# Kernel optimization log

Measured on AMD Instinct MI355X. Metric: run time of the kernel, lower is better.

## Reference

```python
import jax, jax.numpy as jnp
import numpy as np

N = 1024
D = 128  # hidden_dim
NEG = -1e9
LEAK = 0.2


def setup_inputs() -> dict:
    key = jax.random.key(0)
    ks = jax.random.split(key, 10)
    h = jax.random.normal(ks[0], (N, D), dtype=jnp.float32)
    adj = jax.random.randint(ks[1], (N, N), 0, 2, dtype=jnp.int32)  # 0/1 mask
    price_diff = jax.random.normal(ks[2], (N, N), dtype=jnp.float32)
    utilization = jax.random.uniform(ks[3], (N, N), dtype=jnp.float32)
    s = 0.05
    W = jax.random.normal(ks[4], (D, D), dtype=jnp.float32) * s          # W.weight [out,in]
    a = jax.random.normal(ks[5], (2 * D,), dtype=jnp.float32) * s        # attn.weight [1, 2D]
    W1 = jax.random.normal(ks[6], (D, D + 2), dtype=jnp.float32) * s     # mlp[0].weight [D, D+2]
    b1 = jnp.zeros((D,), dtype=jnp.float32)
    W2 = jax.random.normal(ks[7], (D, D), dtype=jnp.float32) * s         # mlp[2].weight [D, D]
    b2 = jnp.zeros((D,), dtype=jnp.float32)
    return {"h": h, "adj": adj, "price_diff": price_diff, "utilization": utilization,
            "W": W, "a": a, "W1": W1, "b1": b1, "W2": W2, "b2": b2}


def reference(h, adj, price_diff, utilization, W, a, W1, b1, W2, b2):
    # Linear projection (no bias): Wh = h @ W^T  -> [N, D]
    Wh = h @ W.T
    # GAT score: e_ij = leaky_relu(a^T [Wh_i || Wh_j]) = leaky_relu(s1_i + s2_j)
    s1 = Wh @ a[:D]          # [N]
    s2 = Wh @ a[D:]          # [N]
    e = jax.nn.leaky_relu(s1[:, None] + s2[None, :], LEAK)  # [N, N]
    mask = adj > 0
    e = jnp.where(mask, e, NEG)
    alpha = jax.nn.softmax(e, axis=-1) * mask.astype(e.dtype)  # zero rows with no neighbors
    # Edge MLP on [Wh_j || price_diff_ij || utilization_ij]
    W1h = W1[:, :D]          # [D, D] part acting on Wh_j
    w_pd = W1[:, D]          # [D]
    w_ut = W1[:, D + 1]      # [D]
    base = Wh @ W1h.T + b1   # [N, D], depends only on source node j
    m1 = jax.nn.relu(base[None, :, :]
                     + price_diff[:, :, None] * w_pd
                     + utilization[:, :, None] * w_ut)          # [N, N, D]
    m2 = m1 @ W2.T + b2                                          # [N, N, D]
    # Attention-weighted aggregation over neighbors j
    out = jnp.einsum('ij,ijd->id', alpha, m2)                    # [N, D]
    return out
```

## Files before the change

### kernel.cpp

```cpp
#include <hip/hip_runtime.h>
#include <hip/hip_bf16.h>

#define N 1024
#define D 128
#define LEAK 0.2f

#define MROWS 2

#define OFF_W2T  0
#define OFF_WPD  16384
#define OFF_WUT  16512
#define OFF_S1   16640
#define OFF_S2   17664
#define OFF_BASE 18688

__global__ __launch_bounds__(256) void prep_base_kernel(
    const float* __restrict__ W, const float* __restrict__ W1,
    const float* __restrict__ W2, const float* __restrict__ a,
    const float* __restrict__ h, const float* __restrict__ b1,
    float* __restrict__ W2t, float* __restrict__ wpd, float* __restrict__ wut,
    float* __restrict__ s1, float* __restrict__ s2, float* __restrict__ base) {
    __shared__ float pool[4160];
    __shared__ float red[4], red2[4];
    int b = blockIdx.x, tid = threadIdx.x;
    if (b < 512) {
        float* hl  = pool;
        float* whl = pool + 256;
        int i0 = b * 2;
        if (tid < 64) ((float4*)hl)[tid] = ((const float4*)(h + i0 * D))[tid];
        __syncthreads();
        int r = tid >> 7, l = tid & 127;
        float u = 0.f;
        #pragma unroll 8
        for (int q = 0; q < D; q += 4) {
            float4 hq = *(const float4*)&hl[r * D + q];
            float4 wq = *(const float4*)&W[l * D + q];
            u = fmaf(hq.x, wq.x, u); u = fmaf(hq.y, wq.y, u);
            u = fmaf(hq.z, wq.z, u); u = fmaf(hq.w, wq.w, u);
        }
        whl[r * D + l] = u;
        __syncthreads();
        {
            int w = tid >> 6, l63 = tid & 63;
            int row = w >> 1, half = w & 1;
            float wh = whl[row * D + half * 64 + l63];
            float p1 = wh * a[half * 64 + l63];
            float p2 = wh * a[D + half * 64 + l63];
            #pragma unroll
            for (int off = 32; off > 0; off >>= 1) {
                p1 += __shfl_xor(p1, off);
                p2 += __shfl_xor(p2, off);
            }
            if (l63 == 0) { red[w] = p1; red2[w] = p2; }
        }
        __syncthreads();
        if (tid < 2) {
            s1[i0 + tid] = red[2 * tid] + red[2 * tid + 1];
            s2[i0 + tid] = red2[2 * tid] + red2[2 * tid + 1];
        }
        float acc = b1[l];
        #pragma unroll 8
        for (int q = 0; q < D; q += 2) {
            float2 wh2 = *(const float2*)&whl[r * D + q];
            float2 x = *(const float2*)&W1[l * (D + 2) + q];
            acc = fmaf(wh2.x, x.x, acc);
            acc = fmaf(wh2.y, x.y, acc);
        }
        base[(i0 + r) * D + l] = acc;
    } else if (b < 516) {
        int kbase = 32 * (b - 512);
        #pragma unroll
        for (int p = 0; p < 16; p++) {
            int idx = tid + p * 256;
            int rd = idx >> 5, cc = idx & 31;
            pool[cc * 129 + rd] = W2[rd * D + kbase + cc];
        }
        __syncthreads();
        #pragma unroll
        for (int p = 0; p < 16; p++) {
            int idx = tid + p * 256;
            int kl = idx >> 7, dd = idx & 127;
            W2t[(kbase + kl) * D + dd] = pool[kl * 129 + dd];
        }
    } else {
        if (tid < 128) wpd[tid] = W1[tid * (D + 2) + D];
        else           wut[tid - 128] = W1[(tid - 128) * (D + 2) + D + 1];
    }
}

__global__ __launch_bounds__(1024, 8) void mega_kernel(
    const float* __restrict__ base, const float* __restrict__ s1,
    const float* __restrict__ s2, const int* __restrict__ adj,
    const float* __restrict__ pd, const float* __restrict__ ut,
    const float* __restrict__ wpd, const float* __restrict__ wut,
    const float* __restrict__ W2t, const float* __restrict__ b2,
    float* __restrict__ out) {
    __shared__ float al[MROWS][N];
    __shared__ float pdl[MROWS][N];
    __shared__ float utl[MROWS][N];
    __shared__ float racc[16][MROWS][D];
    __shared__ float red[16], red2[16], gsum[MROWS];
    __shared__ float tl[MROWS][D];

    const int tid = threadIdx.x;
    const int i0 = blockIdx.x * MROWS;
    const float* pdb = pd + (size_t)i0 * N;
    const float* utb = ut + (size_t)i0 * N;

    {
        int half = tid >> 9, idx = tid & 511;
        const float* src = half ? utb : pdb;
        float* dst = half ? &utl[0][0] : &pdl[0][0];
        ((float4*)dst)[idx] = ((const float4*)src)[idx];
    }

    {
        int r = tid >> 9;
        int i = i0 + r;
        int jb = (tid & 511) * 2;
        float s1i = s1[i];
        float2 sa = *(const float2*)&s2[jb];
        int2 ma = *(const int2*)&adj[i * N + jb];
        float e[2]; int mm[2];
        e[0] = s1i + sa.x; e[1] = s1i + sa.y;
        mm[0] = ma.x; mm[1] = ma.y;
        float mx = -3e38f;
        #pragma unroll
        for (int q = 0; q < 2; q++) {
            e[q] = e[q] > 0.f ? e[q] : LEAK * e[q];
            if (mm[q] > 0) mx = fmaxf(mx, e[q]);
        }
        #pragma unroll
        for (int off = 32; off > 0; off >>= 1) mx = fmaxf(mx, __shfl_xor(mx, off));
        int wid = tid >> 6, lane = tid & 63;
        if (lane == 0) red[wid] = mx;
        __syncthreads();
        {
            float m0 = fmaxf(fmaxf(red[8 * r], red[8 * r + 1]),
                             fmaxf(red[8 * r + 2], red[8 * r + 3]));
            float m1 = fmaxf(fmaxf(red[8 * r + 4], red[8 * r + 5]),
                             fmaxf(red[8 * r + 6], red[8 * r + 7]));
            mx = fmaxf(m0, m1);
        }
        float ev[2]; float sum = 0.f;
        #pragma unroll
        for (int q = 0; q < 2; q++) {
            ev[q] = (mm[q] > 0) ? __expf(e[q] - mx) : 0.f;
            sum += ev[q];
        }
        #pragma unroll
        for (int off = 32; off > 0; off >>= 1) sum += __shfl_xor(sum, off);
        if (lane == 0) red2[wid] = sum;
        __syncthreads();
        sum = red2[8 * r] + red2[8 * r + 1] + red2[8 * r + 2] + red2[8 * r + 3]
            + red2[8 * r + 4] + red2[8 * r + 5] + red2[8 * r + 6] + red2[8 * r + 7];
        float inv = sum > 0.f ? 1.f / sum : 0.f;
        *(float2*)&al[r][jb] = make_float2(ev[0] * inv, ev[1] * inv);
        if ((tid & 511) == 0) gsum[r] = sum;
    }
    __syncthreads();

    const int l16 = tid & 15, g = tid >> 4;
    const int k0a = l16 * 4, k0b = 64 + l16 * 4;
    const float4 wp0 = *(const float4*)&wpd[k0a];
    const float4 wp1 = *(const float4*)&wpd[k0b];
    const float4 wu0 = *(const float4*)&wut[k0a];
    const float4 wu1 = *(const float4*)&wut[k0b];

    float4 a0[MROWS] = {}, a1[MROWS] = {};

    #pragma unroll 2
    for (int c = 0; c < 16; c++) {
        int j = c * 64 + g;
        float4 b0  = *(const float4*)&base[j * D + k0a];
        float4 b1v = *(const float4*)&base[j * D + k0b];
        #pragma unroll
        for (int r = 0; r < MROWS; r++) {
            float spd = pdl[r][j];
            float sut = utl[r][j];
            float sal = al[r][j];
            float v;
            v = fmaxf(fmaf(spd, wp0.x, fmaf(sut, wu0.x, b0.x)), 0.f);  a0[r].x = fmaf(sal, v, a0[r].x);
            v = fmaxf(fmaf(spd, wp0.y, fmaf(sut, wu0.y, b0.y)), 0.f);  a0[r].y = fmaf(sal, v, a0[r].y);
            v = fmaxf(fmaf(spd, wp0.z, fmaf(sut, wu0.z, b0.z)), 0.f);  a0[r].z = fmaf(sal, v, a0[r].z);
            v = fmaxf(fmaf(spd, wp0.w, fmaf(sut, wu0.w, b0.w)), 0.f);  a0[r].w = fmaf(sal, v, a0[r].w);
            v = fmaxf(fmaf(spd, wp1.x, fmaf(sut, wu1.x, b1v.x)), 0.f); a1[r].x = fmaf(sal, v, a1[r].x);
            v = fmaxf(fmaf(spd, wp1.y, fmaf(sut, wu1.y, b1v.y)), 0.f); a1[r].y = fmaf(sal, v, a1[r].y);
            v = fmaxf(fmaf(spd, wp1.z, fmaf(sut, wu1.z, b1v.z)), 0.f); a1[r].z = fmaf(sal, v, a1[r].z);
            v = fmaxf(fmaf(spd, wp1.w, fmaf(sut, wu1.w, b1v.w)), 0.f); a1[r].w = fmaf(sal, v, a1[r].w);
        }
    }

    #pragma unroll
    for (int r = 0; r < MROWS; r++) {
        #pragma unroll
        for (int m = 16; m <= 32; m <<= 1) {
            a0[r].x += __shfl_xor(a0[r].x, m); a0[r].y += __shfl_xor(a0[r].y, m);
            a0[r].z += __shfl_xor(a0[r].z, m); a0[r].w += __shfl_xor(a0[r].w, m);
            a1[r].x += __shfl_xor(a1[r].x, m); a1[r].y += __shfl_xor(a1[r].y, m);
            a1[r].z += __shfl_xor(a1[r].z, m); a1[r].w += __shfl_xor(a1[r].w, m);
        }
    }
    {
        int w = tid >> 6, lane = tid & 63;
        if (lane < 16) {
            #pragma unroll
            for (int r = 0; r < MROWS; r++) {
                *(float4*)&racc[w][r][k0a] = a0[r];
                *(float4*)&racc[w][r][k0b] = a1[r];
            }
        }
    }
    __syncthreads();
    if (tid < 256) {
        int rr = tid >> 7, k = tid & 127;
        float v = 0.f;
        #pragma unroll
        for (int w = 0; w < 16; w++) v += racc[w][rr][k];
        tl[rr][k] = v;
    }
    __syncthreads();
    if (tid < 256) {
        int rr = tid >> 7, d = tid & 127;
        float acc = (gsum[rr] > 0.f) ? b2[d] : 0.f;
        #pragma unroll 8
        for (int k = 0; k < D; k++)
            acc = fmaf(tl[rr][k], W2t[k * D + d], acc);
        out[(i0 + rr) * D + d] = acc;
    }
}

extern "C" void kernel_launch(void* const* d_in, const int* in_sizes, int n_in,
                              void* d_out, int out_size, void* d_ws, size_t ws_size,
                              hipStream_t stream) {
    (void)in_sizes; (void)n_in; (void)out_size; (void)ws_size;
    const float* h   = (const float*)d_in[0];
    const int*   adj = (const int*)d_in[1];
    const float* pd  = (const float*)d_in[2];
    const float* ut  = (const float*)d_in[3];
    const float* W   = (const float*)d_in[4];
    const float* a   = (const float*)d_in[5];
    const float* W1  = (const float*)d_in[6];
    const float* b1  = (const float*)d_in[7];
    const float* W2  = (const float*)d_in[8];
    const float* b2  = (const float*)d_in[9];
    float* out = (float*)d_out;
    float* ws = (float*)d_ws;

    float* W2t   = ws + OFF_W2T;
    float* wpd   = ws + OFF_WPD;
    float* wut   = ws + OFF_WUT;
    float* s1    = ws + OFF_S1;
    float* s2    = ws + OFF_S2;
    float* baseb = ws + OFF_BASE;

    prep_base_kernel<<<517, 256, 0, stream>>>(W, W1, W2, a, h, b1,
                                              W2t, wpd, wut, s1, s2, baseb);
    mega_kernel<<<N / MROWS, 1024, 0, stream>>>(baseb, s1, s2, adj, pd, ut,
                                                wpd, wut, W2t, b2, out);
}
```

Measured before the change: 40.00 us.

## Compact neighbor lists per row and skip masked-out edges in aggregation

Builds a per-row compacted list of neighbor indices in shared memory with a warp prefix scan during the softmax phase. The aggregation loop then iterates only over adjacent j instead of all N, skipping edges whose attention weight is zero (about half for the random mask). In exchange it adds a scan, an extra shared array that lowers occupancy, indirect gathers of base rows, and a separate loop per row, which loses the sharing of each base load across the two rows.

Result: faster. 37.26 us (-6.9%).

```diff
diff --git a/kernel.cpp b/kernel.cpp
--- a/kernel.cpp
+++ b/kernel.cpp
@@ -98,8 +98,10 @@
     __shared__ float al[MROWS][N];
     __shared__ float pdl[MROWS][N];
     __shared__ float utl[MROWS][N];
+    __shared__ int   jlist[MROWS][N];
     __shared__ float racc[16][MROWS][D];
     __shared__ float red[16], red2[16], gsum[MROWS];
+    __shared__ int   wsum[16], gcnt[MROWS];
     __shared__ float tl[MROWS][D];
 
     const int tid = threadIdx.x;
@@ -133,7 +135,15 @@
         #pragma unroll
         for (int off = 32; off > 0; off >>= 1) mx = fmaxf(mx, __shfl_xor(mx, off));
         int wid = tid >> 6, lane = tid & 63;
+        int cl = (mm[0] > 0) + (mm[1] > 0);
+        int incl = cl;
+        #pragma unroll
+        for (int s = 1; s < 64; s <<= 1) {
+            int p = __shfl_up(incl, s);
+            if (lane >= s) incl += p;
+        }
         if (lane == 0) red[wid] = mx;
+        if (lane == 63) wsum[wid] = incl;
         __syncthreads();
         {
             float m0 = fmaxf(fmaxf(red[8 * r], red[8 * r + 1]),
@@ -142,6 +152,17 @@
                              fmaxf(red[8 * r + 6], red[8 * r + 7]));
             mx = fmaxf(m0, m1);
         }
+        int base_off = 0, row_total = 0;
+        #pragma unroll
+        for (int w = 0; w < 8; w++) {
+            int v = wsum[8 * r + w];
+            if (8 * r + w < wid) base_off += v;
+            row_total += v;
+        }
+        int off = base_off + incl - cl;
+        if (mm[0] > 0) jlist[r][off] = jb;
+        if (mm[1] > 0) jlist[r][off + (mm[0] > 0)] = jb + 1;
+        if ((tid & 511) == 0) gcnt[r] = row_total;
         float ev[2]; float sum = 0.f;
         #pragma unroll
         for (int q = 0; q < 2; q++) {
@@ -149,7 +170,7 @@
             sum += ev[q];
         }
         #pragma unroll
-        for (int off = 32; off > 0; off >>= 1) sum += __shfl_xor(sum, off);
+        for (int off2 = 32; off2 > 0; off2 >>= 1) sum += __shfl_xor(sum, off2);
         if (lane == 0) red2[wid] = sum;
         __syncthreads();
         sum = red2[8 * r] + red2[8 * r + 1] + red2[8 * r + 2] + red2[8 * r + 3]
@@ -168,26 +189,50 @@
     const float4 wu1 = *(const float4*)&wut[k0b];
 
     float4 a0[MROWS] = {}, a1[MROWS] = {};
-
-    #pragma unroll 2
-    for (int c = 0; c < 16; c++) {
-        int j = c * 64 + g;
-        float4 b0  = *(const float4*)&base[j * D + k0a];
-        float4 b1v = *(const float4*)&base[j * D + k0b];
-        #pragma unroll
-        for (int r = 0; r < MROWS; r++) {
-            float spd = pdl[r][j];
-            float sut = utl[r][j];
-            float sal = al[r][j];
-            float v;
-            v = fmaxf(fmaf(spd, wp0.x, fmaf(sut, wu0.x, b0.x)), 0.f);  a0[r].x = fmaf(sal, v, a0[r].x);
-            v = fmaxf(fmaf(spd, wp0.y, fmaf(sut, wu0.y, b0.y)), 0.f);  a0[r].y = fmaf(sal, v, a0[r].y);
-            v = fmaxf(fmaf(spd, wp0.z, fmaf(sut, wu0.z, b0.z)), 0.f);  a0[r].z = fmaf(sal, v, a0[r].z);
-            v = fmaxf(fmaf(spd, wp0.w, fmaf(sut, wu0.w, b0.w)), 0.f);  a0[r].w = fmaf(sal, v, a0[r].w);
-            v = fmaxf(fmaf(spd, wp1.x, fmaf(sut, wu1.x, b1v.x)), 0.f); a1[r].x = fmaf(sal, v, a1[r].x);
-            v = fmaxf(fmaf(spd, wp1.y, fmaf(sut, wu1.y, b1v.y)), 0.f); a1[r].y = fmaf(sal, v, a1[r].y);
-            v = fmaxf(fmaf(spd, wp1.z, fmaf(sut, wu1.z, b1v.z)), 0.f); a1[r].z = fmaf(sal, v, a1[r].z);
-            v = fmaxf(fmaf(spd, wp1.w, fmaf(sut, wu1.w, b1v.w)), 0.f); a1[r].w = fmaf(sal, v, a1[r].w);
+    const int gc0 = gcnt[0], gc1 = gcnt[1];
+
+    {
+        int nc = (gc0 + 63) >> 6;
+        #pragma unroll 2
+        for (int c = 0; c < nc; c++) {
+            int idx = c * 64 + g;
+            if (idx < gc0) {
+                int j = jlist[0][idx];
+                float4 b0  = *(const float4*)&base[j * D + k0a];
+                float4 b1v = *(const float4*)&base[j * D + k0b];
+                float spd = pdl[0][j], sut = utl[0][j], sal = al[0][j];
+                float v;
+                v = fmaxf(fmaf(spd, wp0.x, fmaf(sut, wu0.x, b0.x)), 0.f);  a0[0].x = fmaf(sal, v, a0[0].x);
+                v = fmaxf(fmaf(spd, wp0.y, fmaf(sut, wu0.y, b0.y)), 0.f);  a0[0].y = fmaf(sal, v, a0[0].y);
+                v = fmaxf(fmaf(spd, wp0.z, fmaf(sut, wu0.z, b0.z)), 0.f);  a0[0].z = fmaf(sal, v, a0[0].z);
+                v = fmaxf(fmaf(spd, wp0.w, fmaf(sut, wu0.w, b0.w)), 0.f);  a0[0].w = fmaf(sal, v, a0[0].w);
+                v = fmaxf(fmaf(spd, wp1.x, fmaf(sut, wu1.x, b1v.x)), 0.f); a1[0].x = fmaf(sal, v, a1[0].x);
+                v = fmaxf(fmaf(spd, wp1.y, fmaf(sut, wu1.y, b1v.y)), 0.f); a1[0].y = fmaf(sal, v, a1[0].y);
+                v = fmaxf(fmaf(spd, wp1.z, fmaf(sut, wu1.z, b1v.z)), 0.f); a1[0].z = fmaf(sal, v, a1[0].z);
+                v = fmaxf(fmaf(spd, wp1.w, fmaf(sut, wu1.w, b1v.w)), 0.f); a1[0].w = fmaf(sal, v, a1[0].w);
+            }
+        }
+    }
+    {
+        int nc = (gc1 + 63) >> 6;
+        #pragma unroll 2
+        for (int c = 0; c < nc; c++) {
+            int idx = c * 64 + g;
+            if (idx < gc1) {
+                int j = jlist[1][idx];
+                float4 b0  = *(const float4*)&base[j * D + k0a];
+                float4 b1v = *(const float4*)&base[j * D + k0b];
+                float spd = pdl[1][j], sut = utl[1][j], sal = al[1][j];
+                float v;
+                v = fmaxf(fmaf(spd, wp0.x, fmaf(sut, wu0.x, b0.x)), 0.f);  a0[1].x = fmaf(sal, v, a0[1].x);
+                v = fmaxf(fmaf(spd, wp0.y, fmaf(sut, wu0.y, b0.y)), 0.f);  a0[1].y = fmaf(sal, v, a0[1].y);
+                v = fmaxf(fmaf(spd, wp0.z, fmaf(sut, wu0.z, b0.z)), 0.f);  a0[1].z = fmaf(sal, v, a0[1].z);
+                v = fmaxf(fmaf(spd, wp0.w, fmaf(sut, wu0.w, b0.w)), 0.f);  a0[1].w = fmaf(sal, v, a0[1].w);
+                v = fmaxf(fmaf(spd, wp1.x, fmaf(sut, wu1.x, b1v.x)), 0.f); a1[1].x = fmaf(sal, v, a1[1].x);
+                v = fmaxf(fmaf(spd, wp1.y, fmaf(sut, wu1.y, b1v.y)), 0.f); a1[1].y = fmaf(sal, v, a1[1].y);
+                v = fmaxf(fmaf(spd, wp1.z, fmaf(sut, wu1.z, b1v.z)), 0.f); a1[1].z = fmaf(sal, v, a1[1].z);
+                v = fmaxf(fmaf(spd, wp1.w, fmaf(sut, wu1.w, b1v.w)), 0.f); a1[1].w = fmaf(sal, v, a1[1].w);
+            }
         }
     }
 
```
